# Optimization experiments

Hardware: AMD Instinct MI355X
Metric: run time of the kernel (lower is better)

## Reference

```python
import jax, jax.numpy as jnp
import numpy as np

EMB = 1024
HEADS = 16
HEAD_DIM = EMB // HEADS
SEQ = 2048
BATCH = 2
EPS = 1e-5


def gelu_tanh(x):
    # 0.5*x*(1+tanh(sqrt(2/pi)*(x+0.044715*x^3)))
    c = jnp.sqrt(jnp.asarray(2.0 / jnp.pi, x.dtype))
    return 0.5 * x * (1.0 + jnp.tanh(c * (x + 0.044715 * x * x * x)))


def layernorm(x, scale, shift):
    mean = jnp.mean(x, axis=-1, keepdims=True)
    # torch var(unbiased=True) -> ddof=1
    var = jnp.var(x, axis=-1, keepdims=True, ddof=1)
    return scale * (x - mean) / jnp.sqrt(var + EPS) + shift


def setup_inputs() -> dict:
    key = jax.random.key(0)
    ks = jax.random.split(key, 12)
    s = 0.02
    d = {
        "x": jax.random.normal(ks[0], (BATCH, SEQ, EMB), jnp.float32),
        "Wq": jax.random.normal(ks[1], (EMB, EMB), jnp.float32) * s,
        "bq": jnp.zeros((EMB,), jnp.float32),
        "Wk": jax.random.normal(ks[2], (EMB, EMB), jnp.float32) * s,
        "bk": jnp.zeros((EMB,), jnp.float32),
        "Wv": jax.random.normal(ks[3], (EMB, EMB), jnp.float32) * s,
        "bv": jnp.zeros((EMB,), jnp.float32),
        "Wo": jax.random.normal(ks[4], (EMB, EMB), jnp.float32) * s,
        "bo": jnp.zeros((EMB,), jnp.float32),
        "W1": jax.random.normal(ks[5], (EMB, 4 * EMB), jnp.float32) * s,
        "b1": jnp.zeros((4 * EMB,), jnp.float32),
        "W2": jax.random.normal(ks[6], (4 * EMB, EMB), jnp.float32) * s,
        "b2": jnp.zeros((EMB,), jnp.float32),
        "ln1_scale": jnp.ones((EMB,), jnp.float32),
        "ln1_shift": jnp.zeros((EMB,), jnp.float32),
        "ln2_scale": jnp.ones((EMB,), jnp.float32),
        "ln2_shift": jnp.zeros((EMB,), jnp.float32),
    }
    return d


def reference(x, Wq, bq, Wk, bk, Wv, bv, Wo, bo, W1, b1, W2, b2,
              ln1_scale, ln1_shift, ln2_scale, ln2_shift):
    b, n, _ = x.shape

    # --- attention sub-block (pre-norm) ---
    h = layernorm(x, ln1_scale, ln1_shift)
    q = (h @ Wq + bq).reshape(b, n, HEADS, HEAD_DIM).transpose(0, 2, 1, 3)
    k = (h @ Wk + bk).reshape(b, n, HEADS, HEAD_DIM).transpose(0, 2, 1, 3)
    v = (h @ Wv + bv).reshape(b, n, HEADS, HEAD_DIM).transpose(0, 2, 1, 3)

    # explicit O(n^2) scores, as in the source
    scores = jnp.einsum("bhqd,bhkd->bhqk", q, k)
    causal = jnp.triu(jnp.ones((n, n), bool), k=1)  # True above diagonal -> masked
    scores = jnp.where(causal, -jnp.inf, scores)
    weights = jax.nn.softmax(scores / jnp.sqrt(jnp.asarray(HEAD_DIM, x.dtype)), axis=-1)
    ctx = jnp.einsum("bhqk,bhkd->bhqd", weights, v)
    ctx = ctx.transpose(0, 2, 1, 3).reshape(b, n, EMB)
    x = x + (ctx @ Wo + bo)  # dropout is identity (rate 0 / eval)

    # --- FFN sub-block (pre-norm) ---
    h = layernorm(x, ln2_scale, ln2_shift)
    h = gelu_tanh(h @ W1 + b1)
    x = x + (h @ W2 + b2)
    return x
```

## Files before the change

kernel.cpp:

```cpp
#include <hip/hip_runtime.h>
#include <hip/hip_bf16.h>

#define EMB 1024
#define SEQ 2048
#define BATCH 2
#define HEADS 16
#define HDIM 64
#define ROWS (BATCH*SEQ)

typedef __hip_bfloat16 bf16;
typedef __bf16 bf16x8 __attribute__((ext_vector_type(8)));
typedef float f32x4 __attribute__((ext_vector_type(4)));

#define AS1 __attribute__((address_space(1)))
#define AS3 __attribute__((address_space(3)))

__device__ __forceinline__ void load_lds16(const void* g, void* l) {
    __builtin_amdgcn_global_load_lds((const AS1 void*)g, (AS3 void*)l, 16, 0, 0);
}

__device__ __forceinline__ float gelu_f(float x) {
    float y = 1.5957691216057308f * (x + 0.044715f * x * x * x);
    return x / (1.0f + __expf(-y));
}

__global__ void transpose_cast_kernel(const float* __restrict__ in, bf16* __restrict__ out,
                                      int R, int C) {
    __shared__ bf16 tile[32][33];
    int tx = threadIdx.x, ty = threadIdx.y;
    int c0 = blockIdx.x * 32, r0 = blockIdx.y * 32;
    for (int i = ty; i < 32; i += 8)
        tile[i][tx] = (bf16)in[(size_t)(r0 + i) * C + c0 + tx];
    __syncthreads();
    for (int i = ty; i < 32; i += 8)
        out[(size_t)(c0 + i) * R + r0 + tx] = tile[tx][i];
}

__global__ void transpose_cast4_kernel(const float* __restrict__ w0, const float* __restrict__ w1,
                                       const float* __restrict__ w2, const float* __restrict__ w3,
                                       bf16* __restrict__ o0, bf16* __restrict__ o1,
                                       bf16* __restrict__ o2, bf16* __restrict__ o3) {
    __shared__ bf16 tile[32][33];
    int z = blockIdx.z;
    const float* in = (z == 0) ? w0 : (z == 1) ? w1 : (z == 2) ? w2 : w3;
    bf16* out = (z == 0) ? o0 : (z == 1) ? o1 : (z == 2) ? o2 : o3;
    int tx = threadIdx.x, ty = threadIdx.y;
    int c0 = blockIdx.x * 32, r0 = blockIdx.y * 32;
    for (int i = ty; i < 32; i += 8)
        tile[i][tx] = (bf16)in[(size_t)(r0 + i) * 1024 + c0 + tx];
    __syncthreads();
    for (int i = ty; i < 32; i += 8)
        out[(size_t)(c0 + i) * 1024 + r0 + tx] = tile[tx][i];
}

__global__ void transpose_v_kernel(const bf16* __restrict__ v, bf16* __restrict__ vt) {
    __shared__ bf16 tile[32][33];
    int tx = threadIdx.x, ty = threadIdx.y;
    int bh = blockIdx.z;
    const bf16* in = v + (size_t)(bh >> 4) * SEQ * EMB + (bh & 15) * HDIM;
    bf16* out = vt + (size_t)bh * HDIM * SEQ;
    int s0 = blockIdx.x * 32, d0 = blockIdx.y * 32;
    for (int i = ty; i < 32; i += 8)
        tile[i][tx] = in[(size_t)(s0 + i) * EMB + d0 + tx];
    __syncthreads();
    for (int i = ty; i < 32; i += 8)
        out[(size_t)(d0 + i) * SEQ + s0 + tx] = tile[tx][i];
}

__global__ __launch_bounds__(256) void layernorm_kernel(const float* __restrict__ x,
                                                        bf16* __restrict__ out,
                                                        const float* __restrict__ scale,
                                                        const float* __restrict__ shift) {
    int row = blockIdx.x;
    int t = threadIdx.x;
    const float* xr = x + (size_t)row * EMB;
    float v[4];
    float s = 0.f, s2 = 0.f;
#pragma unroll
    for (int i = 0; i < 4; i++) {
        v[i] = xr[t + 256 * i];
        s += v[i];
        s2 += v[i] * v[i];
    }
#pragma unroll
    for (int off = 32; off > 0; off >>= 1) {
        s += __shfl_down(s, off);
        s2 += __shfl_down(s2, off);
    }
    __shared__ float sh[8];
    __shared__ float stats[2];
    int lane = t & 63, wid = t >> 6;
    if (lane == 0) { sh[wid] = s; sh[wid + 4] = s2; }
    __syncthreads();
    if (t == 0) {
        float ts = sh[0] + sh[1] + sh[2] + sh[3];
        float ts2 = sh[4] + sh[5] + sh[6] + sh[7];
        float mean = ts / (float)EMB;
        float var = (ts2 - (float)EMB * mean * mean) / (float)(EMB - 1);
        stats[0] = mean;
        stats[1] = rsqrtf(var + 1e-5f);
    }
    __syncthreads();
    float mean = stats[0], inv = stats[1];
#pragma unroll
    for (int i = 0; i < 4; i++) {
        int c = t + 256 * i;
        float y = (v[i] - mean) * inv * scale[c] + shift[c];
        out[(size_t)row * EMB + c] = (bf16)y;
    }
}

__device__ __forceinline__ void swz32(int id, int& bx, int& by) {
    int xcd = id & 7, m = id >> 3;
    by = xcd + 8 * (m & 3);
    bx = m >> 2;
}
__device__ __forceinline__ void swz64(int id, int& bx, int& by) {
    int xcd = id & 7, m = id >> 3;
    by = xcd + 8 * (m & 3) + 32 * (m >> 6);
    bx = (m >> 2) & 15;
}

template <int ACT, int RES, int OUTF>
__global__ __launch_bounds__(256) void gemm_kernel(const bf16* __restrict__ A,
                                                   const bf16* __restrict__ BT,
                                                   void* __restrict__ Cout,
                                                   const float* __restrict__ bias,
                                                   const float* __restrict__ res,
                                                   int M, int N, int K) {
    __shared__ __align__(16) bf16 lA[2][128 * 32];
    __shared__ __align__(16) bf16 lB[2][128 * 32];
    int tid = threadIdx.x;
    int wave = tid >> 6, lane = tid & 63;
    int bx, by;
    swz32(blockIdx.x, bx, by);
    int m0 = by * 128, n0 = bx * 128;
    int wm = (wave >> 1) * 64, wn = (wave & 1) * 64;
    f32x4 acc[4][4] = {};

    int srow = wave * 16 + (lane >> 2);
    int skc = (lane & 3) * 8;
    const bf16* Ag = A + (size_t)(m0 + srow) * K + skc;
    const bf16* Bg = BT + (size_t)(n0 + srow) * K + skc;
    size_t woff = (size_t)(wave * 16) * 32;

    const int an = lane & 15;
    const int ak = (lane >> 4) * 8;

    load_lds16(Ag, lA[0] + woff);
    load_lds16(Ag + (size_t)64 * K, lA[0] + woff + 64 * 32);
    load_lds16(Bg, lB[0] + woff);
    load_lds16(Bg + (size_t)64 * K, lB[0] + woff + 64 * 32);

    int nsteps = K >> 5;
    for (int t = 0; t < nsteps; t++) {
        int buf = t & 1;
        asm volatile("s_waitcnt vmcnt(0)" ::: "memory");
        __syncthreads();
        if (t + 1 < nsteps) {
            int k0 = (t + 1) * 32;
            load_lds16(Ag + k0, lA[buf ^ 1] + woff);
            load_lds16(Ag + (size_t)64 * K + k0, lA[buf ^ 1] + woff + 64 * 32);
            load_lds16(Bg + k0, lB[buf ^ 1] + woff);
            load_lds16(Bg + (size_t)64 * K + k0, lB[buf ^ 1] + woff + 64 * 32);
        }
        bf16x8 af[4], bfv[4];
#pragma unroll
        for (int i = 0; i < 4; i++)
            af[i] = *(const bf16x8*)(lA[buf] + (wm + 16 * i + an) * 32 + ak);
#pragma unroll
        for (int j = 0; j < 4; j++)
            bfv[j] = *(const bf16x8*)(lB[buf] + (wn + 16 * j + an) * 32 + ak);
#pragma unroll
        for (int i = 0; i < 4; i++)
#pragma unroll
            for (int j = 0; j < 4; j++)
                acc[i][j] = __builtin_amdgcn_mfma_f32_16x16x32_bf16(af[i], bfv[j], acc[i][j], 0, 0, 0);
    }
#pragma unroll
    for (int j = 0; j < 4; j++) {
        int col = n0 + wn + 16 * j + an;
        float bv = bias[col];
#pragma unroll
        for (int i = 0; i < 4; i++) {
#pragma unroll
            for (int r = 0; r < 4; r++) {
                int row = m0 + wm + 16 * i + (lane >> 4) * 4 + r;
                float vx = acc[i][j][r] + bv;
                if (ACT == 1) vx = gelu_f(vx);
                size_t idx = (size_t)row * N + col;
                if (RES == 2) vx += res[idx];
                if (OUTF == 0) ((bf16*)Cout)[idx] = (bf16)vx;
                else ((float*)Cout)[idx] = vx;
            }
        }
    }
}

template <int RES, int OUTF>
__global__ __launch_bounds__(256) void gemm64_kernel(const bf16* __restrict__ A,
                                                     const bf16* __restrict__ BT,
                                                     void* __restrict__ Cout,
                                                     const float* __restrict__ bias,
                                                     const float* __restrict__ res,
                                                     int M, int N, int K) {
    __shared__ __align__(16) bf16 lA[2][2][64 * 32];
    __shared__ __align__(16) bf16 lB[2][2][64 * 32];
    int tid = threadIdx.x;
    int wave = tid >> 6, lane = tid & 63;
    int bx, by;
    swz64(blockIdx.x, bx, by);
    int m0 = by * 64, n0 = bx * 64;
    int wm = (wave >> 1) * 32, wn = (wave & 1) * 32;
    f32x4 acc[2][2] = {};

    int srow = wave * 16 + (lane >> 2);
    int skc = (lane & 3) * 8;
    const bf16* Ag = A + (size_t)(m0 + srow) * K + skc;
    const bf16* Bg = BT + (size_t)(n0 + srow) * K + skc;
    size_t woff = (size_t)(wave * 16) * 32;

    const int an = lane & 15;
    const int ak = (lane >> 4) * 8;

    load_lds16(Ag, &lA[0][0][woff]);
    load_lds16(Ag + 32, &lA[0][1][woff]);
    load_lds16(Bg, &lB[0][0][woff]);
    load_lds16(Bg + 32, &lB[0][1][woff]);

    int nsteps = K >> 6;
    for (int t = 0; t < nsteps; t++) {
        int buf = t & 1;
        asm volatile("s_waitcnt vmcnt(0)" ::: "memory");
        __syncthreads();
        if (t + 1 < nsteps) {
            int k0 = (t + 1) * 64;
            load_lds16(Ag + k0, &lA[buf ^ 1][0][woff]);
            load_lds16(Ag + k0 + 32, &lA[buf ^ 1][1][woff]);
            load_lds16(Bg + k0, &lB[buf ^ 1][0][woff]);
            load_lds16(Bg + k0 + 32, &lB[buf ^ 1][1][woff]);
        }
#pragma unroll
        for (int h = 0; h < 2; h++) {
            bf16x8 af[2], bfv[2];
#pragma unroll
            for (int i = 0; i < 2; i++)
                af[i] = *(const bf16x8*)(&lA[buf][h][(wm + 16 * i + an) * 32 + ak]);
#pragma unroll
            for (int j = 0; j < 2; j++)
                bfv[j] = *(const bf16x8*)(&lB[buf][h][(wn + 16 * j + an) * 32 + ak]);
#pragma unroll
            for (int i = 0; i < 2; i++)
#pragma unroll
                for (int j = 0; j < 2; j++)
                    acc[i][j] = __builtin_amdgcn_mfma_f32_16x16x32_bf16(af[i], bfv[j], acc[i][j], 0, 0, 0);
        }
    }
#pragma unroll
    for (int j = 0; j < 2; j++) {
        int col = n0 + wn + 16 * j + an;
        float bv = bias[col];
#pragma unroll
        for (int i = 0; i < 2; i++) {
#pragma unroll
            for (int r = 0; r < 4; r++) {
                int row = m0 + wm + 16 * i + (lane >> 4) * 4 + r;
                float vx = acc[i][j][r] + bv;
                size_t idx = (size_t)row * N + col;
                if (RES == 2) vx += res[idx];
                if (OUTF == 0) ((bf16*)Cout)[idx] = (bf16)vx;
                else ((float*)Cout)[idx] = vx;
            }
        }
    }
}

__global__ __launch_bounds__(256) void gemm_qkv_kernel(const bf16* __restrict__ A,
                                                       const bf16* __restrict__ BT,
                                                       bf16* __restrict__ qo,
                                                       bf16* __restrict__ ko,
                                                       bf16* __restrict__ vo,
                                                       const float* __restrict__ bq,
                                                       const float* __restrict__ bk,
                                                       const float* __restrict__ bv) {
    const int K = EMB;
    __shared__ __align__(16) bf16 lA[2][128 * 32];
    __shared__ __align__(16) bf16 lB[2][128 * 32];
    int tid = threadIdx.x;
    int wave = tid >> 6, lane = tid & 63;
    int bx, by;
    swz32(blockIdx.x, bx, by);
    int m0 = by * 128, n0 = bx * 128;
    int wm = (wave >> 1) * 64, wn = (wave & 1) * 64;
    f32x4 acc[4][4] = {};

    int srow = wave * 16 + (lane >> 2);
    int skc = (lane & 3) * 8;
    const bf16* Ag = A + (size_t)(m0 + srow) * K + skc;
    const bf16* Bg = BT + (size_t)(n0 + srow) * K + skc;
    size_t woff = (size_t)(wave * 16) * 32;

    const int an = lane & 15;
    const int ak = (lane >> 4) * 8;

    load_lds16(Ag, lA[0] + woff);
    load_lds16(Ag + (size_t)64 * K, lA[0] + woff + 64 * 32);
    load_lds16(Bg, lB[0] + woff);
    load_lds16(Bg + (size_t)64 * K, lB[0] + woff + 64 * 32);

    const int nsteps = K >> 5;
    for (int t = 0; t < nsteps; t++) {
        int buf = t & 1;
        asm volatile("s_waitcnt vmcnt(0)" ::: "memory");
        __syncthreads();
        if (t + 1 < nsteps) {
            int k0 = (t + 1) * 32;
            load_lds16(Ag + k0, lA[buf ^ 1] + woff);
            load_lds16(Ag + (size_t)64 * K + k0, lA[buf ^ 1] + woff + 64 * 32);
            load_lds16(Bg + k0, lB[buf ^ 1] + woff);
            load_lds16(Bg + (size_t)64 * K + k0, lB[buf ^ 1] + woff + 64 * 32);
        }
        bf16x8 af[4], bfv[4];
#pragma unroll
        for (int i = 0; i < 4; i++)
            af[i] = *(const bf16x8*)(lA[buf] + (wm + 16 * i + an) * 32 + ak);
#pragma unroll
        for (int j = 0; j < 4; j++)
            bfv[j] = *(const bf16x8*)(lB[buf] + (wn + 16 * j + an) * 32 + ak);
#pragma unroll
        for (int i = 0; i < 4; i++)
#pragma unroll
            for (int j = 0; j < 4; j++)
                acc[i][j] = __builtin_amdgcn_mfma_f32_16x16x32_bf16(af[i], bfv[j], acc[i][j], 0, 0, 0);
    }
#pragma unroll
    for (int j = 0; j < 4; j++) {
        int col = n0 + wn + 16 * j + an;
        int region = col >> 10;
        int c = col & 1023;
        const float* bias = (region == 0) ? bq : (region == 1) ? bk : bv;
        bf16* outp = (region == 0) ? qo : (region == 1) ? ko : vo;
        float scl = (region == 0) ? 0.125f : 1.0f;
        float bvv = bias[c];
#pragma unroll
        for (int i = 0; i < 4; i++) {
#pragma unroll
            for (int r = 0; r < 4; r++) {
                int row = m0 + wm + 16 * i + (lane >> 4) * 4 + r;
                float vx = (acc[i][j][r] + bvv) * scl;
                outp[(size_t)row * EMB + c] = (bf16)vx;
            }
        }
    }
}

__global__ __launch_bounds__(256) void attn_kernel(const bf16* __restrict__ q,
                                                   const bf16* __restrict__ k,
                                                   const bf16* __restrict__ vt,
                                                   bf16* __restrict__ ctx) {
    __shared__ __align__(16) bf16 ksm[2][2048];
    __shared__ __align__(16) bf16 vsm[2][2048];
    __shared__ __align__(16) bf16 pbuf[4][16][32];
    int tid = threadIdx.x;
    int wave = tid >> 6, lane = tid & 63;
    int id = blockIdx.x;
    int bh = id >> 5;
    int bx = ((id & 31) + bh) & 31;
    int b = bh >> 4, h = bh & 15;
    int q0 = bx * 64 + wave * 16;
    const bf16* qp = q + (size_t)b * SEQ * EMB + h * HDIM;
    const bf16* kp = k + (size_t)b * SEQ * EMB + h * HDIM;
    const bf16* vp = vt + (size_t)bh * HDIM * SEQ;

    int an = lane & 15;
    int aq = lane >> 4;
    bf16x8 qf0 = *(const bf16x8*)(qp + (size_t)(q0 + an) * EMB + aq * 8);
    bf16x8 qf1 = *(const bf16x8*)(qp + (size_t)(q0 + an) * EMB + 32 + aq * 8);
    f32x4 o[4] = {};
    float lp[4] = {0.f, 0.f, 0.f, 0.f};

    const bf16* kg = kp + (size_t)((wave & 1) * 16 + (lane >> 2)) * EMB + ((wave & 2) ? 32 : 0) + (lane & 3) * 8;
    const bf16* vg = vp + (size_t)(wave * 16 + (lane >> 2)) * SEQ + (lane & 3) * 8;

    int nsteps = 2 * bx + 2;
    load_lds16(kg, (char*)ksm[0] + wave * 1024);
    load_lds16(vg, (char*)vsm[0] + wave * 1024);

    for (int t = 0; t < nsteps; t++) {
        int buf = t & 1;
        asm volatile("s_waitcnt vmcnt(0)" ::: "memory");
        __syncthreads();
        if (t + 1 < nsteps) {
            int kvn = (t + 1) * 32;
            load_lds16(kg + (size_t)kvn * EMB, (char*)ksm[buf ^ 1] + wave * 1024);
            load_lds16(vg + kvn, (char*)vsm[buf ^ 1] + wave * 1024);
        }
        const char* kb = (const char*)ksm[buf];
        bf16x8 kf0 = *(const bf16x8*)(kb + an * 64 + aq * 16);
        bf16x8 kf1 = *(const bf16x8*)(kb + 2048 + an * 64 + aq * 16);
        bf16x8 kf2 = *(const bf16x8*)(kb + (16 + an) * 64 + aq * 16);
        bf16x8 kf3 = *(const bf16x8*)(kb + 2048 + (16 + an) * 64 + aq * 16);
        f32x4 s0 = {}, s1 = {};
        s0 = __builtin_amdgcn_mfma_f32_16x16x32_bf16(qf0, kf0, s0, 0, 0, 0);
        s0 = __builtin_amdgcn_mfma_f32_16x16x32_bf16(qf1, kf1, s0, 0, 0, 0);
        s1 = __builtin_amdgcn_mfma_f32_16x16x32_bf16(qf0, kf2, s1, 0, 0, 0);
        s1 = __builtin_amdgcn_mfma_f32_16x16x32_bf16(qf1, kf3, s1, 0, 0, 0);
        int kv = t * 32;
        if (t < nsteps - 2) {
#pragma unroll
            for (int r = 0; r < 4; r++) {
                float p0 = __expf(s0[r]);
                float p1 = __expf(s1[r]);
                lp[r] += p0 + p1;
                pbuf[wave][aq * 4 + r][an] = (bf16)p0;
                pbuf[wave][aq * 4 + r][16 + an] = (bf16)p1;
            }
        } else {
#pragma unroll
            for (int r = 0; r < 4; r++) {
                int row = q0 + aq * 4 + r;
                float p0 = (kv + an > row) ? 0.f : __expf(s0[r]);
                float p1 = (kv + 16 + an > row) ? 0.f : __expf(s1[r]);
                lp[r] += p0 + p1;
                pbuf[wave][aq * 4 + r][an] = (bf16)p0;
                pbuf[wave][aq * 4 + r][16 + an] = (bf16)p1;
            }
        }
        asm volatile("s_waitcnt lgkmcnt(0)" ::: "memory");
        bf16x8 pa = *(const bf16x8*)(&pbuf[wave][an][aq * 8]);
        const char* vb = (const char*)vsm[buf];
#pragma unroll
        for (int dt = 0; dt < 4; dt++) {
            bf16x8 vf = *(const bf16x8*)(vb + (dt * 16 + an) * 64 + aq * 16);
            o[dt] = __builtin_amdgcn_mfma_f32_16x16x32_bf16(pa, vf, o[dt], 0, 0, 0);
        }
    }
#pragma unroll
    for (int r = 0; r < 4; r++) {
        float v = lp[r];
        v += __shfl_xor(v, 1);
        v += __shfl_xor(v, 2);
        v += __shfl_xor(v, 4);
        v += __shfl_xor(v, 8);
        lp[r] = v;
    }
#pragma unroll
    for (int dt = 0; dt < 4; dt++) {
#pragma unroll
        for (int r = 0; r < 4; r++) {
            int row = q0 + aq * 4 + r;
            int col = h * HDIM + dt * 16 + an;
            ctx[((size_t)b * SEQ + row) * EMB + col] = (bf16)(o[dt][r] / lp[r]);
        }
    }
}

extern "C" void kernel_launch(void* const* d_in, const int* in_sizes, int n_in,
                              void* d_out, int out_size, void* d_ws, size_t ws_size,
                              hipStream_t stream) {
    const float* x = (const float*)d_in[0];
    const float* Wq = (const float*)d_in[1];
    const float* bq = (const float*)d_in[2];
    const float* Wk = (const float*)d_in[3];
    const float* bk = (const float*)d_in[4];
    const float* Wv = (const float*)d_in[5];
    const float* bv = (const float*)d_in[6];
    const float* Wo = (const float*)d_in[7];
    const float* bo = (const float*)d_in[8];
    const float* W1 = (const float*)d_in[9];
    const float* b1 = (const float*)d_in[10];
    const float* W2 = (const float*)d_in[11];
    const float* b2 = (const float*)d_in[12];
    const float* ln1s = (const float*)d_in[13];
    const float* ln1b = (const float*)d_in[14];
    const float* ln2s = (const float*)d_in[15];
    const float* ln2b = (const float*)d_in[16];
    float* out = (float*)d_out;

    char* ws = (char*)d_ws;
    const size_t MB = 1ull << 20;
    bf16* WqT = (bf16*)(ws + 0 * MB);
    bf16* WkT = (bf16*)(ws + 2 * MB);
    bf16* WvT = (bf16*)(ws + 4 * MB);
    bf16* WoT = (bf16*)(ws + 6 * MB);
    bf16* W1T = (bf16*)(ws + 8 * MB);
    bf16* W2T = (bf16*)(ws + 16 * MB);
    bf16* hbuf = (bf16*)(ws + 24 * MB);
    bf16* qbuf = (bf16*)(ws + 32 * MB);
    bf16* kbuf = (bf16*)(ws + 40 * MB);
    bf16* vbuf = (bf16*)(ws + 48 * MB);
    bf16* vtb = (bf16*)(ws + 56 * MB);
    bf16* ctxb = (bf16*)(ws + 64 * MB);
    float* x1 = (float*)(ws + 72 * MB);
    bf16* hff = (bf16*)(ws + 32 * MB);

    dim3 tb(32, 8);
    transpose_cast4_kernel<<<dim3(32, 32, 4), tb, 0, stream>>>(Wq, Wk, Wv, Wo, WqT, WkT, WvT, WoT);
    transpose_cast_kernel<<<dim3(128, 32), tb, 0, stream>>>(W1, W1T, 1024, 4096);
    transpose_cast_kernel<<<dim3(32, 128), tb, 0, stream>>>(W2, W2T, 4096, 1024);

    layernorm_kernel<<<ROWS, 256, 0, stream>>>(x, hbuf, ln1s, ln1b);

    gemm_qkv_kernel<<<768, 256, 0, stream>>>(hbuf, WqT, qbuf, kbuf, vbuf, bq, bk, bv);

    transpose_v_kernel<<<dim3(64, 2, 32), tb, 0, stream>>>(vbuf, vtb);

    attn_kernel<<<1024, 256, 0, stream>>>(qbuf, kbuf, vtb, ctxb);

    gemm64_kernel<2, 1><<<1024, 256, 0, stream>>>(ctxb, WoT, x1, bo, x, ROWS, EMB, EMB);

    layernorm_kernel<<<ROWS, 256, 0, stream>>>(x1, hbuf, ln2s, ln2b);

    gemm_kernel<1, 0, 0><<<1024, 256, 0, stream>>>(hbuf, W1T, hff, b1, nullptr, ROWS, 4 * EMB, EMB);

    gemm64_kernel<2, 1><<<1024, 256, 0, stream>>>(hff, W2T, out, b2, x1, ROWS, EMB, 4 * EMB);
}
```

Measured before the change: 379.3 us.

## Triple-buffer LDS tiles with prefetch distance two in GEMM and attention loops

Each GEMM variant and the attention kernel move from double to triple LDS buffering. Loads are now issued two K-steps ahead, and the wait uses a partial vmcnt instead of draining all outstanding global-to-LDS loads every iteration. The goal is to hide more global memory latency behind the MFMA work. The cost is 50% more shared memory per block, which may lower occupancy. The hand-written vmcnt/lgkmcnt barrier also has to be exactly right for LDS-direct loads to stay correct.

```diff
diff --git a/kernel.cpp b/kernel.cpp
--- a/kernel.cpp
+++ b/kernel.cpp
@@ -18,6 +18,9 @@
 __device__ __forceinline__ void load_lds16(const void* g, void* l) {
     __builtin_amdgcn_global_load_lds((const AS1 void*)g, (AS3 void*)l, 16, 0, 0);
 }
+
+#define WAITV(N) asm volatile("s_waitcnt vmcnt(" #N ")" ::: "memory")
+#define BAR_LGKM() asm volatile("s_waitcnt lgkmcnt(0)\n\ts_barrier" ::: "memory")
 
 __device__ __forceinline__ float gelu_f(float x) {
     float y = 1.5957691216057308f * (x + 0.044715f * x * x * x);
@@ -128,8 +131,8 @@
                                                    const float* __restrict__ bias,
                                                    const float* __restrict__ res,
                                                    int M, int N, int K) {
-    __shared__ __align__(16) bf16 lA[2][128 * 32];
-    __shared__ __align__(16) bf16 lB[2][128 * 32];
+    __shared__ __align__(16) bf16 lA[3][128 * 32];
+    __shared__ __align__(16) bf16 lB[3][128 * 32];
     int tid = threadIdx.x;
     int wave = tid >> 6, lane = tid & 63;
     int bx, by;
@@ -147,22 +150,28 @@
     const int an = lane & 15;
     const int ak = (lane >> 4) * 8;
 
-    load_lds16(Ag, lA[0] + woff);
-    load_lds16(Ag + (size_t)64 * K, lA[0] + woff + 64 * 32);
-    load_lds16(Bg, lB[0] + woff);
-    load_lds16(Bg + (size_t)64 * K, lB[0] + woff + 64 * 32);
+#pragma unroll
+    for (int p = 0; p < 2; p++) {
+        int k0 = p * 32;
+        load_lds16(Ag + k0, lA[p] + woff);
+        load_lds16(Ag + (size_t)64 * K + k0, lA[p] + woff + 64 * 32);
+        load_lds16(Bg + k0, lB[p] + woff);
+        load_lds16(Bg + (size_t)64 * K + k0, lB[p] + woff + 64 * 32);
+    }
 
     int nsteps = K >> 5;
     for (int t = 0; t < nsteps; t++) {
-        int buf = t & 1;
-        asm volatile("s_waitcnt vmcnt(0)" ::: "memory");
-        __syncthreads();
-        if (t + 1 < nsteps) {
-            int k0 = (t + 1) * 32;
-            load_lds16(Ag + k0, lA[buf ^ 1] + woff);
-            load_lds16(Ag + (size_t)64 * K + k0, lA[buf ^ 1] + woff + 64 * 32);
-            load_lds16(Bg + k0, lB[buf ^ 1] + woff);
-            load_lds16(Bg + (size_t)64 * K + k0, lB[buf ^ 1] + woff + 64 * 32);
+        int buf = t % 3;
+        if (t + 1 < nsteps) WAITV(4);
+        else                WAITV(0);
+        BAR_LGKM();
+        if (t + 2 < nsteps) {
+            int k0 = (t + 2) * 32;
+            int wb = (t + 2) % 3;
+            load_lds16(Ag + k0, lA[wb] + woff);
+            load_lds16(Ag + (size_t)64 * K + k0, lA[wb] + woff + 64 * 32);
+            load_lds16(Bg + k0, lB[wb] + woff);
+            load_lds16(Bg + (size_t)64 * K + k0, lB[wb] + woff + 64 * 32);
         }
         bf16x8 af[4], bfv[4];
 #pragma unroll
@@ -204,8 +213,8 @@
                                                      const float* __restrict__ bias,
                                                      const float* __restrict__ res,
                                                      int M, int N, int K) {
-    __shared__ __align__(16) bf16 lA[2][2][64 * 32];
-    __shared__ __align__(16) bf16 lB[2][2][64 * 32];
+    __shared__ __align__(16) bf16 lA[3][2][64 * 32];
+    __shared__ __align__(16) bf16 lB[3][2][64 * 32];
     int tid = threadIdx.x;
     int wave = tid >> 6, lane = tid & 63;
     int bx, by;
@@ -223,22 +232,28 @@
     const int an = lane & 15;
     const int ak = (lane >> 4) * 8;
 
-    load_lds16(Ag, &lA[0][0][woff]);
-    load_lds16(Ag + 32, &lA[0][1][woff]);
-    load_lds16(Bg, &lB[0][0][woff]);
-    load_lds16(Bg + 32, &lB[0][1][woff]);
+#pragma unroll
+    for (int p = 0; p < 2; p++) {
+        int k0 = p * 64;
+        load_lds16(Ag + k0, &lA[p][0][woff]);
+        load_lds16(Ag + k0 + 32, &lA[p][1][woff]);
+        load_lds16(Bg + k0, &lB[p][0][woff]);
+        load_lds16(Bg + k0 + 32, &lB[p][1][woff]);
+    }
 
     int nsteps = K >> 6;
     for (int t = 0; t < nsteps; t++) {
-        int buf = t & 1;
-        asm volatile("s_waitcnt vmcnt(0)" ::: "memory");
-        __syncthreads();
-        if (t + 1 < nsteps) {
-            int k0 = (t + 1) * 64;
-            load_lds16(Ag + k0, &lA[buf ^ 1][0][woff]);
-            load_lds16(Ag + k0 + 32, &lA[buf ^ 1][1][woff]);
-            load_lds16(Bg + k0, &lB[buf ^ 1][0][woff]);
-            load_lds16(Bg + k0 + 32, &lB[buf ^ 1][1][woff]);
+        int buf = t % 3;
+        if (t + 1 < nsteps) WAITV(4);
+        else                WAITV(0);
+        BAR_LGKM();
+        if (t + 2 < nsteps) {
+            int k0 = (t + 2) * 64;
+            int wb = (t + 2) % 3;
+            load_lds16(Ag + k0, &lA[wb][0][woff]);
+            load_lds16(Ag + k0 + 32, &lA[wb][1][woff]);
+            load_lds16(Bg + k0, &lB[wb][0][woff]);
+            load_lds16(Bg + k0 + 32, &lB[wb][1][woff]);
         }
 #pragma unroll
         for (int h = 0; h < 2; h++) {
@@ -284,8 +299,8 @@
                                                        const float* __restrict__ bk,
                                                        const float* __restrict__ bv) {
     const int K = EMB;
-    __shared__ __align__(16) bf16 lA[2][128 * 32];
-    __shared__ __align__(16) bf16 lB[2][128 * 32];
+    __shared__ __align__(16) bf16 lA[3][128 * 32];
+    __shared__ __align__(16) bf16 lB[3][128 * 32];
     int tid = threadIdx.x;
     int wave = tid >> 6, lane = tid & 63;
     int bx, by;
@@ -303,22 +318,28 @@
     const int an = lane & 15;
     const int ak = (lane >> 4) * 8;
 
-    load_lds16(Ag, lA[0] + woff);
-    load_lds16(Ag + (size_t)64 * K, lA[0] + woff + 64 * 32);
-    load_lds16(Bg, lB[0] + woff);
-    load_lds16(Bg + (size_t)64 * K, lB[0] + woff + 64 * 32);
+#pragma unroll
+    for (int p = 0; p < 2; p++) {
+        int k0 = p * 32;
+        load_lds16(Ag + k0, lA[p] + woff);
+        load_lds16(Ag + (size_t)64 * K + k0, lA[p] + woff + 64 * 32);
+        load_lds16(Bg + k0, lB[p] + woff);
+        load_lds16(Bg + (size_t)64 * K + k0, lB[p] + woff + 64 * 32);
+    }
 
     const int nsteps = K >> 5;
     for (int t = 0; t < nsteps; t++) {
-        int buf = t & 1;
-        asm volatile("s_waitcnt vmcnt(0)" ::: "memory");
-        __syncthreads();
-        if (t + 1 < nsteps) {
-            int k0 = (t + 1) * 32;
-            load_lds16(Ag + k0, lA[buf ^ 1] + woff);
-            load_lds16(Ag + (size_t)64 * K + k0, lA[buf ^ 1] + woff + 64 * 32);
-            load_lds16(Bg + k0, lB[buf ^ 1] + woff);
-            load_lds16(Bg + (size_t)64 * K + k0, lB[buf ^ 1] + woff + 64 * 32);
+        int buf = t % 3;
+        if (t + 1 < nsteps) WAITV(4);
+        else                WAITV(0);
+        BAR_LGKM();
+        if (t + 2 < nsteps) {
+            int k0 = (t + 2) * 32;
+            int wb = (t + 2) % 3;
+            load_lds16(Ag + k0, lA[wb] + woff);
+            load_lds16(Ag + (size_t)64 * K + k0, lA[wb] + woff + 64 * 32);
+            load_lds16(Bg + k0, lB[wb] + woff);
+            load_lds16(Bg + (size_t)64 * K + k0, lB[wb] + woff + 64 * 32);
         }
         bf16x8 af[4], bfv[4];
 #pragma unroll
@@ -358,8 +379,8 @@
                                                    const bf16* __restrict__ k,
                                                    const bf16* __restrict__ vt,
                                                    bf16* __restrict__ ctx) {
-    __shared__ __align__(16) bf16 ksm[2][2048];
-    __shared__ __align__(16) bf16 vsm[2][2048];
+    __shared__ __align__(16) bf16 ksm[3][2048];
+    __shared__ __align__(16) bf16 vsm[3][2048];
     __shared__ __align__(16) bf16 pbuf[4][16][32];
     int tid = threadIdx.x;
     int wave = tid >> 6, lane = tid & 63;
@@ -385,15 +406,19 @@
     int nsteps = 2 * bx + 2;
     load_lds16(kg, (char*)ksm[0] + wave * 1024);
     load_lds16(vg, (char*)vsm[0] + wave * 1024);
+    load_lds16(kg + (size_t)32 * EMB, (char*)ksm[1] + wave * 1024);
+    load_lds16(vg + 32, (char*)vsm[1] + wave * 1024);
 
     for (int t = 0; t < nsteps; t++) {
-        int buf = t & 1;
-        asm volatile("s_waitcnt vmcnt(0)" ::: "memory");
-        __syncthreads();
-        if (t + 1 < nsteps) {
-            int kvn = (t + 1) * 32;
-            load_lds16(kg + (size_t)kvn * EMB, (char*)ksm[buf ^ 1] + wave * 1024);
-            load_lds16(vg + kvn, (char*)vsm[buf ^ 1] + wave * 1024);
+        int buf = t % 3;
+        if (t + 1 < nsteps) WAITV(2);
+        else                WAITV(0);
+        BAR_LGKM();
+        if (t + 2 < nsteps) {
+            int kvn = (t + 2) * 32;
+            int wb = (t + 2) % 3;
+            load_lds16(kg + (size_t)kvn * EMB, (char*)ksm[wb] + wave * 1024);
+            load_lds16(vg + kvn, (char*)vsm[wb] + wave * 1024);
         }
         const char* kb = (const char*)ksm[buf];
         bf16x8 kf0 = *(const bf16x8*)(kb + an * 64 + aq * 16);
```

Measured after the change: 430.8 us. 1.14x slower.
